# Optimization experiments

Measured on AMD Instinct MI355X. Metric: run time of the kernel, lower is better.

## Reference

```python
import jax, jax.numpy as jnp
import numpy as np

B, IN, H, MID = 16384, 256, 512, 64
GRID_SIZE, ORDER = 5, 3
GRID_LO, GRID_HI = -1.0, 1.0
NB = GRID_SIZE + ORDER  # 8 spline basis functions per input feature
LN_EPS = 1e-5


def make_grid(in_features):
    h = (GRID_HI - GRID_LO) / GRID_SIZE
    g = np.arange(-ORDER, GRID_SIZE + ORDER + 1, dtype=np.float32) * h + GRID_LO
    return jnp.asarray(np.tile(g, (in_features, 1)))  # (in, grid_size + 2*order + 1)


def layer_norm(x, g, b):
    mu = jnp.mean(x, axis=-1, keepdims=True)
    var = jnp.var(x, axis=-1, keepdims=True)
    return (x - mu) * jax.lax.rsqrt(var + LN_EPS) * g + b


def b_splines(x, grid):
    # x: (B, in), grid: (in, G). Cox-de Boor recursion (efficient-kan convention).
    xe = x[:, :, None]
    bases = ((xe >= grid[:, :-1]) & (xe < grid[:, 1:])).astype(x.dtype)
    for k in range(1, ORDER + 1):
        left = (xe - grid[:, :-(k + 1)]) / (grid[:, k:-1] - grid[:, :-(k + 1)])
        right = (grid[:, k + 1:] - xe) / (grid[:, k + 1:] - grid[:, 1:-k])
        bases = left * bases[:, :, :-1] + right * bases[:, :, 1:]
    return bases  # (B, in, NB)


def kan_linear(x, base_w, spline_w, scaler, grid):
    # base path: silu(x) @ W_base^T ; spline path: B-spline bases contracted with scaled spline weights
    base = jax.nn.silu(x) @ base_w.T
    bs = b_splines(x, grid)
    spline = jnp.einsum('bik,oik->bo', bs, spline_w * scaler[:, :, None])
    return base + spline


def setup_inputs() -> dict:
    key = jax.random.key(0)
    ks = jax.random.split(key, 24)

    def n(k, shape, fan_in):
        return jax.random.normal(k, shape, dtype=jnp.float32) / np.sqrt(fan_in)

    H2 = 2 * H
    return {
        'x': jax.random.normal(ks[0], (B, IN), jnp.float32),
        'h_prev': jax.random.normal(ks[1], (B, H), jnp.float32),
        'ip_w': n(ks[2], (H, IN), IN), 'ip_b': jnp.zeros((H,), jnp.float32),
        'rg_w': n(ks[3], (H, H2), H2), 'rg_b': jnp.zeros((H,), jnp.float32),
        'rg_g': jnp.ones((H,), jnp.float32), 'rg_beta': jnp.zeros((H,), jnp.float32),
        'ug_w': n(ks[4], (H, H2), H2), 'ug_b': jnp.zeros((H,), jnp.float32),
        'ug_g': jnp.ones((H,), jnp.float32), 'ug_beta': jnp.zeros((H,), jnp.float32),
        'k1_base': n(ks[5], (MID, H2), H2),
        'k1_spline': n(ks[6], (MID, H2, NB), H2) * 0.1,
        'k1_scaler': n(ks[7], (MID, H2), H2) + 1.0,
        'grid1': make_grid(H2),
        'k2_base': n(ks[8], (H, MID), MID),
        'k2_spline': n(ks[9], (H, MID, NB), MID) * 0.1,
        'k2_scaler': n(ks[10], (H, MID), MID) + 1.0,
        'grid2': make_grid(MID),
        'cn_g': jnp.ones((H,), jnp.float32), 'cn_b': jnp.zeros((H,), jnp.float32),
        'rp_w': n(ks[11], (H, H2), H2), 'rp_b': jnp.zeros((H,), jnp.float32),
    }


def reference(x, h_prev, ip_w, ip_b, rg_w, rg_b, rg_g, rg_beta, ug_w, ug_b, ug_g, ug_beta,
              k1_base, k1_spline, k1_scaler, grid1, k2_base, k2_spline, k2_scaler, grid2,
              cn_g, cn_b, rp_w, rp_b):
    x_proj = x @ ip_w.T + ip_b
    combined = jnp.concatenate([x_proj, h_prev], axis=1)  # (B, 2H)
    # reset gate is computed in the original forward but never used; kept for faithfulness
    reset = jnp.tanh(layer_norm(combined @ rg_w.T + rg_b, rg_g, rg_beta))  # noqa: F841
    update = jax.nn.sigmoid(layer_norm(combined @ ug_w.T + ug_b, ug_g, ug_beta))
    # KAN candidate: [2H] -> 64 -> H
    mid = kan_linear(combined, k1_base, k1_spline, k1_scaler, grid1)
    h_cand = kan_linear(mid, k2_base, k2_spline, k2_scaler, grid2)
    residual = combined @ rp_w.T + rp_b
    h_cand = layer_norm(h_cand + residual, cn_g, cn_b)
    h_cand = layer_norm(h_cand, cn_g, cn_b)  # same LayerNorm applied twice, as in source
    h_cand = jax.nn.silu(h_cand)
    h_t = (1.0 - update) * h_prev + update * h_cand
    return h_t
```

## Files before the change

kernel.cpp:

```cpp
#include <hip/hip_runtime.h>
#include <hip/hip_bf16.h>

#define BATCH 16384

typedef __attribute__((ext_vector_type(8))) short short8;
typedef __attribute__((ext_vector_type(4))) float f32x4;

typedef const __attribute__((address_space(1))) uint* gas_t;
typedef __attribute__((address_space(3))) uint* las_t;

__device__ __forceinline__ void gl_lds16(const void* g, void* l) {
    __builtin_amdgcn_global_load_lds((gas_t)g, (las_t)l, 16, 0, 0);
}

__device__ __forceinline__ float bf2f(uint u) { union { uint u; float f; } v; v.u = u << 16; return v.f; }
__device__ __forceinline__ ushort f2bf(float f) {
    union { float f; uint u; } v; v.f = f;
    uint r = v.u + 0x7fffu + ((v.u >> 16) & 1u);
    return (ushort)(r >> 16);
}
__device__ __forceinline__ uint pack2(float a, float b) { return (uint)f2bf(a) | ((uint)f2bf(b) << 16); }
__device__ __forceinline__ uint pack_trunc(float lo, float hi) {
    return __builtin_amdgcn_perm(__float_as_uint(hi), __float_as_uint(lo), 0x07060302u);
}
__device__ __forceinline__ float sigmoidf_(float x) { return __builtin_amdgcn_rcpf(1.0f + __expf(-x)); }
__device__ __forceinline__ float siluf_(float x)    { return x * sigmoidf_(x); }

__device__ __forceinline__ void bases_packed(float x, float g0, float inv_h, uint o[4]) {
    float u = (x - g0) * inv_h;
    float fl = floorf(u);
    float f = u - fl;
    float f2 = f * f, f3 = f2 * f;
    float Ca = f3 * (1.0f / 6.0f);
    float Cb = (1.0f / 6.0f) + 0.5f * (f + f2 - f3);
    float Cc = (2.0f / 3.0f) + 0.5f * f3 - f2;
    float Cd = (1.0f / 6.0f) + 0.5f * (f2 - f) - f3 * (1.0f / 6.0f);
    int t0 = (int)fl;
    t0 = max(-8, min(t0, 19));
    uint dlo = pack_trunc(Cd, Cc);
    uint dhi = pack_trunc(Cb, Ca);
    unsigned long long D = (unsigned long long)dlo | ((unsigned long long)dhi << 32);
    int sp = t0 * 16 - 48;
    unsigned long long l1 = D << (sp & 63);
    unsigned long long r1 = D >> ((-sp) & 63);
    unsigned long long r2 = D >> ((64 - sp) & 63);
    unsigned long long l2 = D << ((sp - 64) & 63);
    unsigned long long lo = (sp >= 0) ? (sp < 64 ? l1 : 0ull) : (sp > -64 ? r1 : 0ull);
    unsigned long long hi = (sp > 0 && sp < 128) ? (sp < 64 ? r2 : l2) : 0ull;
    o[0] = (uint)lo; o[1] = (uint)(lo >> 32); o[2] = (uint)hi; o[3] = (uint)(hi >> 32);
}

__global__ __launch_bounds__(256) void prep_all(const float* __restrict__ ip_w, const float* __restrict__ ug_w,
                                                const float* __restrict__ rp,  const float* __restrict__ k2b,
                                                const float* __restrict__ k2s, const float* __restrict__ k2sc,
                                                const float* __restrict__ k1b, const float* __restrict__ k1s,
                                                const float* __restrict__ k1sc,
                                                ushort* __restrict__ ipw, ushort* __restrict__ ugw,
                                                ushort* __restrict__ wcat, ushort* __restrict__ w1aug) {
    int t = blockIdx.x * 256 + threadIdx.x;
    if (t < 131072) { ipw[t] = f2bf(ip_w[t]); return; }
    t -= 131072;
    if (t < 524288) { ugw[t] = f2bf(ug_w[t]); return; }
    t -= 524288;
    if (t < 819200) {
        int n = t / 1600, c = t % 1600; float v;
        if (c < 1024) v = rp[n * 1024 + c];
        else if (c < 1088) v = k2b[n * 64 + (c - 1024)];
        else { int i = (c - 1088) >> 3, k = (c - 1088) & 7; v = k2s[(n * 64 + i) * 8 + k] * k2sc[n * 64 + i]; }
        wcat[t] = f2bf(v); return;
    }
    t -= 819200;
    if (t < 589824) {
        int n = t / 9216, c = t % 9216; float v;
        if (c < 1024) v = k1b[n * 1024 + c];
        else { int i = (c - 1024) >> 3, k = (c - 1024) & 7; v = k1s[(n * 1024 + i) * 8 + k] * k1sc[n * 1024 + i]; }
        w1aug[t] = f2bf(v);
    }
}

__global__ __launch_bounds__(256) void copy_h_sil(const float* __restrict__ hp,
                                                  ushort* __restrict__ acat, ushort* __restrict__ ssw) {
    int t = blockIdx.x * 256 + threadIdx.x;
    int b = t >> 6, j = (t & 63) * 8;
    const float4* s = (const float4*)(hp + (size_t)b * 512 + j);
    float4 a = s[0], c = s[1];
    uint4 o; o.x = pack2(a.x, a.y); o.y = pack2(a.z, a.w); o.z = pack2(c.x, c.y); o.w = pack2(c.z, c.w);
    *(uint4*)(acat + (size_t)b * 1600 + 512 + j) = o;
    uint4 q; q.x = pack2(siluf_(a.x), siluf_(a.y)); q.y = pack2(siluf_(a.z), siluf_(a.w));
    q.z = pack2(siluf_(c.x), siluf_(c.y)); q.w = pack2(siluf_(c.z), siluf_(c.w));
    *(uint4*)(ssw + (size_t)b * 1024 + 512 + j) = q;
}

__global__ __launch_bounds__(256) void gemm_mfma(const ushort* __restrict__ A, int lda,
                                                 const ushort* __restrict__ Wt, int ldw,
                                                 const float* __restrict__ bias,
                                                 ushort* __restrict__ C, int ldc, int K) {
    __shared__ ushort As[2][128 * 64];
    __shared__ ushort Bs[2][128 * 64];
    const int tid = threadIdx.x;
    const int w = tid >> 6, lane = tid & 63;
    const int fr = lane & 15, fq = lane >> 4;
    const int m0 = blockIdx.x * 128, n0 = blockIdx.y * 128;
    const int wm = w & 1, wn = w >> 1;

    const int srow8 = lane >> 3;
    const int scol  = ((lane & 7) ^ srow8) << 3;
    const ushort* gA[4]; const ushort* gB[4]; int fa[4];
#pragma unroll
    for (int j = 0; j < 4; ++j) {
        int rowj = (j * 4 + w) * 8 + srow8;
        fa[j] = (j * 4 + w) * 512 + lane * 8;
        gA[j] = A  + (size_t)(m0 + rowj) * lda + scol;
        gB[j] = Wt + (size_t)(n0 + rowj) * ldw + scol;
    }
    const int nt = K / 64;
#pragma unroll
    for (int j = 0; j < 4; ++j) {
        gl_lds16(gA[j], &As[0][fa[j]]); gl_lds16(gB[j], &Bs[0][fa[j]]);
        gA[j] += 64; gB[j] += 64;
    }
    f32x4 acc[4][4] = {};
    int cur = 0;
    for (int t = 0; t < nt; ++t) {
        __syncthreads();
        if (t + 1 < nt) {
#pragma unroll
            for (int j = 0; j < 4; ++j) {
                gl_lds16(gA[j], &As[cur ^ 1][fa[j]]); gl_lds16(gB[j], &Bs[cur ^ 1][fa[j]]);
                gA[j] += 64; gB[j] += 64;
            }
        }
#pragma unroll
        for (int s = 0; s < 2; ++s) {
            const int csw = ((s * 4 + fq) ^ (fr & 7)) << 3;
            short8 af[4], bv[4];
#pragma unroll
            for (int mi = 0; mi < 4; ++mi)
                af[mi] = *(const short8*)(&As[cur][(wm * 64 + mi * 16 + fr) * 64 + csw]);
#pragma unroll
            for (int ni = 0; ni < 4; ++ni)
                bv[ni] = *(const short8*)(&Bs[cur][(wn * 64 + ni * 16 + fr) * 64 + csw]);
#pragma unroll
            for (int mi = 0; mi < 4; ++mi)
#pragma unroll
                for (int ni = 0; ni < 4; ++ni)
                    acc[mi][ni] = __builtin_amdgcn_mfma_f32_16x16x32_bf16(af[mi], bv[ni], acc[mi][ni], 0, 0, 0);
        }
        cur ^= 1;
    }
#pragma unroll
    for (int mi = 0; mi < 4; ++mi) {
#pragma unroll
        for (int ni = 0; ni < 4; ++ni) {
            int n = n0 + wn * 64 + ni * 16 + fr;
            float bvs = bias[n];
#pragma unroll
            for (int r = 0; r < 4; ++r) {
                int m = m0 + wm * 64 + mi * 16 + fq * 4 + r;
                C[(size_t)m * ldc + n] = f2bf(acc[mi][ni][r] + bvs);
            }
        }
    }
}

__global__ __launch_bounds__(256) void gemm_ip(const float* __restrict__ X,
                                               const ushort* __restrict__ Wt,
                                               const float* __restrict__ bias,
                                               ushort* __restrict__ acat,
                                               ushort* __restrict__ ssw) {
    __shared__ ushort As[2][128 * 64];
    __shared__ ushort Bs[2][128 * 64];
    const int tid = threadIdx.x;
    const int w = tid >> 6, lane = tid & 63;
    const int fr = lane & 15, fq = lane >> 4;
    const int m0 = blockIdx.x * 128, n0 = blockIdx.y * 128;
    const int wm = w & 1, wn = w >> 1;

    const int srow8 = lane >> 3;
    const int scol = ((lane & 7) ^ srow8) << 3;
    const ushort* gB[4]; int fa[4];
#pragma unroll
    for (int j = 0; j < 4; ++j) {
        int rowj = (j * 4 + w) * 8 + srow8;
        fa[j] = (j * 4 + w) * 512 + lane * 8;
        gB[j] = Wt + (size_t)(n0 + rowj) * 256 + scol;
    }
    const float* gA[4]; int ar[4];
#pragma unroll
    for (int j = 0; j < 4; ++j) {
        int rj = j * 32 + (tid >> 3);
        int lc = (tid & 7) ^ (rj & 7);
        ar[j] = rj * 64 + (tid & 7) * 8;
        gA[j] = X + (size_t)(m0 + rj) * 256 + lc * 8;
    }
    float4 va[4], vb[4];
#pragma unroll
    for (int j = 0; j < 4; ++j) { gl_lds16(gB[j], &Bs[0][fa[j]]); gB[j] += 64; }
#pragma unroll
    for (int j = 0; j < 4; ++j) { va[j] = *(const float4*)gA[j]; vb[j] = *(const float4*)(gA[j] + 4); gA[j] += 64; }
#pragma unroll
    for (int j = 0; j < 4; ++j) {
        uint4 o; o.x = pack2(va[j].x, va[j].y); o.y = pack2(va[j].z, va[j].w);
        o.z = pack2(vb[j].x, vb[j].y); o.w = pack2(vb[j].z, vb[j].w);
        *(uint4*)&As[0][ar[j]] = o;
    }
    f32x4 acc[4][4] = {};
    int cur = 0;
    for (int t = 0; t < 4; ++t) {
        __syncthreads();
        if (t < 3) {
#pragma unroll
            for (int j = 0; j < 4; ++j) { gl_lds16(gB[j], &Bs[cur ^ 1][fa[j]]); gB[j] += 64; }
#pragma unroll
            for (int j = 0; j < 4; ++j) { va[j] = *(const float4*)gA[j]; vb[j] = *(const float4*)(gA[j] + 4); gA[j] += 64; }
        }
#pragma unroll
        for (int s = 0; s < 2; ++s) {
            const int csw = ((s * 4 + fq) ^ (fr & 7)) << 3;
            short8 af[4], bv[4];
#pragma unroll
            for (int mi = 0; mi < 4; ++mi)
                af[mi] = *(const short8*)(&As[cur][(wm * 64 + mi * 16 + fr) * 64 + csw]);
#pragma unroll
            for (int ni = 0; ni < 4; ++ni)
                bv[ni] = *(const short8*)(&Bs[cur][(wn * 64 + ni * 16 + fr) * 64 + csw]);
#pragma unroll
            for (int mi = 0; mi < 4; ++mi)
#pragma unroll
                for (int ni = 0; ni < 4; ++ni)
                    acc[mi][ni] = __builtin_amdgcn_mfma_f32_16x16x32_bf16(af[mi], bv[ni], acc[mi][ni], 0, 0, 0);
        }
        if (t < 3) {
#pragma unroll
            for (int j = 0; j < 4; ++j) {
                uint4 o; o.x = pack2(va[j].x, va[j].y); o.y = pack2(va[j].z, va[j].w);
                o.z = pack2(vb[j].x, vb[j].y); o.w = pack2(vb[j].z, vb[j].w);
                *(uint4*)&As[cur ^ 1][ar[j]] = o;
            }
        }
        cur ^= 1;
    }
#pragma unroll
    for (int mi = 0; mi < 4; ++mi) {
#pragma unroll
        for (int ni = 0; ni < 4; ++ni) {
            int n = n0 + wn * 64 + ni * 16 + fr;
            float bvs = bias[n];
#pragma unroll
            for (int r = 0; r < 4; ++r) {
                int m = m0 + wm * 64 + mi * 16 + fq * 4 + r;
                float val = acc[mi][ni][r] + bvs;
                acat[(size_t)m * 1600 + n] = f2bf(val);
                ssw[(size_t)m * 1024 + n] = f2bf(siluf_(val));
            }
        }
    }
}

__global__ __launch_bounds__(256) void kan1_mfma(const ushort* __restrict__ acat,
                                                 const ushort* __restrict__ ssw,
                                                 const ushort* __restrict__ w1aug,
                                                 const float* __restrict__ grid1,
                                                 float* __restrict__ midp) {
    __shared__ ushort As[2][64 * 64];
    __shared__ ushort Bs[2][64 * 64];
    const int tid = threadIdx.x;
    const int w = tid >> 6, lane = tid & 63;
    const int fr = lane & 15, fq = lane >> 4;
    const int m0 = blockIdx.x * 64;
    const int kb = blockIdx.y;
    const float g0 = grid1[0];
    const float inv_h = 1.0f / (grid1[1] - g0);

    const int srow = tid >> 3, sc = tid & 7;
    const int xr = srow & 7;
    const int lc8 = (sc ^ xr) << 3;
    const ushort* swA0 = ssw + (size_t)(m0 + srow) * 1024 + lc8;
    const ushort* swA1 = ssw + (size_t)(m0 + srow + 32) * 1024 + lc8;
    const ushort* wB0  = w1aug + (size_t)srow * 9216 + lc8;
    const ushort* wB1  = w1aug + (size_t)(srow + 32) * 9216 + lc8;
    const ushort* aRow0 = acat + (size_t)(m0 + srow) * 1600;
    const ushort* aRow1 = acat + (size_t)(m0 + srow + 32) * 1600;
    const int wpo = srow * 64 + lc8;
    const int wm = w & 1, wn = w >> 1;

    f32x4 acc[2][2] = {};
    {
        int c = kb * 128;
        gl_lds16(wB0 + c, &Bs[0][tid * 8]); gl_lds16(wB1 + c, &Bs[0][2048 + tid * 8]);
        gl_lds16(swA0 + c, &As[0][tid * 8]); gl_lds16(swA1 + c, &As[0][2048 + tid * 8]);
    }
    int cur = 0;
    for (int s = 0; s < 18; ++s) {
        __syncthreads();
        if (s + 1 < 18) {
            int c = (s + 1 < 2) ? kb * 128 + (s + 1) * 64 : 1024 + kb * 1024 + (s - 1) * 64;
            gl_lds16(wB0 + c, &Bs[cur ^ 1][tid * 8]);
            gl_lds16(wB1 + c, &Bs[cur ^ 1][2048 + tid * 8]);
            if (s + 1 < 2) {
                gl_lds16(swA0 + c, &As[cur ^ 1][tid * 8]);
                gl_lds16(swA1 + c, &As[cur ^ 1][2048 + tid * 8]);
            } else {
                int i = ((c - 1024) >> 3) + sc;
                float x0 = bf2f((uint)aRow0[i]);
                float x1 = bf2f((uint)aRow1[i]);
                uint o0[4], o1[4];
                bases_packed(x0, g0, inv_h, o0);
                bases_packed(x1, g0, inv_h, o1);
                uint4 q0; q0.x = o0[0]; q0.y = o0[1]; q0.z = o0[2]; q0.w = o0[3];
                uint4 q1; q1.x = o1[0]; q1.y = o1[1]; q1.z = o1[2]; q1.w = o1[3];
                *(uint4*)&As[cur ^ 1][wpo] = q0;
                *(uint4*)&As[cur ^ 1][2048 + wpo] = q1;
            }
        }
#pragma unroll
        for (int s2 = 0; s2 < 2; ++s2) {
            short8 af[2], bv[2];
#pragma unroll
            for (int mi = 0; mi < 2; ++mi) {
                int arow = wm * 32 + mi * 16 + fr;
                af[mi] = *(const short8*)(&As[cur][arow * 64 + (((s2 * 4 + fq) ^ (arow & 7)) << 3)]);
            }
#pragma unroll
            for (int ni = 0; ni < 2; ++ni) {
                int brow = wn * 32 + ni * 16 + fr;
                bv[ni] = *(const short8*)(&Bs[cur][brow * 64 + (((s2 * 4 + fq) ^ (brow & 7)) << 3)]);
            }
#pragma unroll
            for (int mi = 0; mi < 2; ++mi)
#pragma unroll
                for (int ni = 0; ni < 2; ++ni)
                    acc[mi][ni] = __builtin_amdgcn_mfma_f32_16x16x32_bf16(af[mi], bv[ni], acc[mi][ni], 0, 0, 0);
        }
        cur ^= 1;
    }
    float* outp = midp + (size_t)kb * (BATCH * 64);
#pragma unroll
    for (int mi = 0; mi < 2; ++mi)
#pragma unroll
        for (int ni = 0; ni < 2; ++ni)
#pragma unroll
            for (int r = 0; r < 4; ++r)
                outp[(size_t)(m0 + wm * 32 + mi * 16 + fq * 4 + r) * 64 + wn * 32 + ni * 16 + fr] = acc[mi][ni][r];
}

__global__ __launch_bounds__(256) void bs2_kernel(const float* __restrict__ midp,
                                                  const float* __restrict__ grid2,
                                                  ushort* __restrict__ acat) {
    int t = blockIdx.x * 256 + threadIdx.x;
    if (t >= BATCH * 64) return;
    float x = 0.0f;
#pragma unroll
    for (int p = 0; p < 8; ++p) x += midp[(size_t)p * (BATCH * 64) + t];
    int b = t >> 6, i = t & 63;
    float g0 = grid2[0], inv_h = 1.0f / (grid2[1] - g0);
    acat[(size_t)b * 1600 + 1024 + i] = f2bf(siluf_(x));
    uint o[4];
    bases_packed(x, g0, inv_h, o);
    uint4 o4; o4.x = o[0]; o4.y = o[1]; o4.z = o[2]; o4.w = o[3];
    *(uint4*)&acat[(size_t)b * 1600 + 1088 + i * 8] = o4;
}

__device__ __forceinline__ void block_reduce_2(float& a, float& b, float (*red)[4]) {
#pragma unroll
    for (int off = 32; off; off >>= 1) {
        a += __shfl_xor(a, off, 64);
        b += __shfl_xor(b, off, 64);
    }
    int lane = threadIdx.x & 63, wid = threadIdx.x >> 6;
    if (lane == 0) { red[0][wid] = a; red[1][wid] = b; }
    __syncthreads();
    a = red[0][0] + red[0][1] + red[0][2] + red[0][3];
    b = red[1][0] + red[1][1] + red[1][2] + red[1][3];
}

__global__ __launch_bounds__(256) void final2(const ushort* __restrict__ ug,
                                              const ushort* __restrict__ hcb,
                                              const float* __restrict__ hprev,
                                              const float* __restrict__ ug_g,
                                              const float* __restrict__ ug_beta,
                                              const float* __restrict__ cg,
                                              const float* __restrict__ cb,
                                              float* __restrict__ out) {
    int row = blockIdx.x, tid = threadIdx.x;
    __shared__ float rA[2][4], rB[2][4], rC[2][4];
    float u0 = bf2f((uint)ug[(size_t)row * 512 + tid]);
    float u1 = bf2f((uint)ug[(size_t)row * 512 + tid + 256]);
    float h0 = bf2f((uint)hcb[(size_t)row * 512 + tid]);
    float h1 = bf2f((uint)hcb[(size_t)row * 512 + tid + 256]);
    float s = u0 + u1, ss = u0 * u0 + u1 * u1;
    block_reduce_2(s, ss, rA);
    float mu = s * (1.0f / 512.0f);
    float var = ss * (1.0f / 512.0f) - mu * mu;
    float r = rsqrtf(var + 1e-5f);
    float uu0 = sigmoidf_((u0 - mu) * r * ug_g[tid] + ug_beta[tid]);
    float uu1 = sigmoidf_((u1 - mu) * r * ug_g[tid + 256] + ug_beta[tid + 256]);
    float cg0 = cg[tid], cg1 = cg[tid + 256], cb0 = cb[tid], cb1 = cb[tid + 256];
    float s2 = h0 + h1, ss2 = h0 * h0 + h1 * h1;
    block_reduce_2(s2, ss2, rB);
    float mu2 = s2 * (1.0f / 512.0f);
    float var2 = ss2 * (1.0f / 512.0f) - mu2 * mu2;
    float r2 = rsqrtf(var2 + 1e-5f);
    float w0 = (h0 - mu2) * r2 * cg0 + cb0;
    float w1 = (h1 - mu2) * r2 * cg1 + cb1;
    float s3 = w0 + w1, ss3 = w0 * w0 + w1 * w1;
    block_reduce_2(s3, ss3, rC);
    float mu3 = s3 * (1.0f / 512.0f);
    float var3 = ss3 * (1.0f / 512.0f) - mu3 * mu3;
    float r3 = rsqrtf(var3 + 1e-5f);
    float c0 = siluf_((w0 - mu3) * r3 * cg0 + cb0);
    float c1 = siluf_((w1 - mu3) * r3 * cg1 + cb1);
    size_t o0 = (size_t)row * 512 + tid, o1 = o0 + 256;
    float hp0 = hprev[o0], hp1 = hprev[o1];
    out[o0] = (1.0f - uu0) * hp0 + uu0 * c0;
    out[o1] = (1.0f - uu1) * hp1 + uu1 * c1;
}

extern "C" void kernel_launch(void* const* d_in, const int* in_sizes, int n_in,
                              void* d_out, int out_size, void* d_ws, size_t ws_size,
                              hipStream_t stream) {
    const float* x        = (const float*)d_in[0];
    const float* h_prev   = (const float*)d_in[1];
    const float* ip_w     = (const float*)d_in[2];
    const float* ip_b     = (const float*)d_in[3];
    const float* ug_w     = (const float*)d_in[8];
    const float* ug_b     = (const float*)d_in[9];
    const float* ug_g     = (const float*)d_in[10];
    const float* ug_beta  = (const float*)d_in[11];
    const float* k1_base  = (const float*)d_in[12];
    const float* k1_spline= (const float*)d_in[13];
    const float* k1_scaler= (const float*)d_in[14];
    const float* grid1    = (const float*)d_in[15];
    const float* k2_base  = (const float*)d_in[16];
    const float* k2_spline= (const float*)d_in[17];
    const float* k2_scaler= (const float*)d_in[18];
    const float* grid2    = (const float*)d_in[19];
    const float* cn_g     = (const float*)d_in[20];
    const float* cn_b     = (const float*)d_in[21];
    const float* rp_w     = (const float*)d_in[22];
    const float* rp_b     = (const float*)d_in[23];
    float* out = (float*)d_out;
    char* W = (char*)d_ws;

    ushort* Acat    = (ushort*)(W);
    ushort* ug_bf   = (ushort*)(W + 52428800);
    ushort* silu_sw = (ushort*)(W + 69206016);
    float*  midp    = (float*) (W + 102760448);
    ushort* hc_bf   = (ushort*)(W + 102760448);
    ushort* ipw_bf  = (ushort*)(W + 136314880);
    ushort* ugw_bf  = (ushort*)(W + 136577024);
    ushort* wcat    = (ushort*)(W + 137625600);
    ushort* w1aug   = (ushort*)(W + 139264000);

    hipLaunchKernelGGL(prep_all, dim3(8064), dim3(256), 0, stream,
                       ip_w, ug_w, rp_w, k2_base, k2_spline, k2_scaler,
                       k1_base, k1_spline, k1_scaler, ipw_bf, ugw_bf, wcat, w1aug);
    hipLaunchKernelGGL(copy_h_sil, dim3(4096), dim3(256), 0, stream, h_prev, Acat, silu_sw);

    hipLaunchKernelGGL(gemm_ip, dim3(BATCH / 128, 4), dim3(256), 0, stream,
                       x, ipw_bf, ip_b, Acat, silu_sw);

    hipLaunchKernelGGL(gemm_mfma, dim3(BATCH / 128, 4), dim3(256), 0, stream,
                       Acat, 1600, ugw_bf, 1024, ug_b, ug_bf, 512, 1024);

    hipLaunchKernelGGL(kan1_mfma, dim3(BATCH / 64, 8), dim3(256), 0, stream,
                       Acat, silu_sw, w1aug, grid1, midp);
    hipLaunchKernelGGL(bs2_kernel, dim3(BATCH * 64 / 256), dim3(256), 0, stream, midp, grid2, Acat);

    hipLaunchKernelGGL(gemm_mfma, dim3(BATCH / 128, 4), dim3(256), 0, stream,
                       Acat, 1600, wcat, 1600, rp_b, hc_bf, 512, 1600);

    hipLaunchKernelGGL(final2, dim3(BATCH), dim3(256), 0, stream, ug_bf, hc_bf, h_prev, ug_g, ug_beta, cn_g, cn_b, out);
}
```

Baseline: 175.2 us.

## Shrink GEMM N-tile to 64, restage KAN1 pipeline, read bf16 h_prev in final

The shared bf16 MFMA GEMM uses 128x64 tiles instead of 128x128, doubling the grid to improve occupancy and CU fill for the N=512 outputs. The KAN layer-1 kernel preloads its input scalars into registers up front and runs an explicitly unrolled double-buffered schedule instead of loading them per stage. The final kernel reads h_prev from the bf16 concatenated buffer rather than the fp32 input, cutting bytes read. This lowers the precision of the residual h_prev term, and the smaller tile re-reads A more often.

```diff
diff --git a/kernel.cpp b/kernel.cpp
--- a/kernel.cpp
+++ b/kernel.cpp
@@ -91,59 +91,65 @@
     *(uint4*)(ssw + (size_t)b * 1024 + 512 + j) = q;
 }
 
-__global__ __launch_bounds__(256) void gemm_mfma(const ushort* __restrict__ A, int lda,
-                                                 const ushort* __restrict__ Wt, int ldw,
-                                                 const float* __restrict__ bias,
-                                                 ushort* __restrict__ C, int ldc, int K) {
+__global__ __launch_bounds__(256) void gemm_n64(const ushort* __restrict__ A, int lda,
+                                                const ushort* __restrict__ Wt, int ldw,
+                                                const float* __restrict__ bias,
+                                                ushort* __restrict__ C, int ldc, int K) {
     __shared__ ushort As[2][128 * 64];
-    __shared__ ushort Bs[2][128 * 64];
+    __shared__ ushort Bs[2][64 * 64];
     const int tid = threadIdx.x;
     const int w = tid >> 6, lane = tid & 63;
     const int fr = lane & 15, fq = lane >> 4;
-    const int m0 = blockIdx.x * 128, n0 = blockIdx.y * 128;
+    const int m0 = blockIdx.x * 128, n0 = blockIdx.y * 64;
     const int wm = w & 1, wn = w >> 1;
-
-    const int srow8 = lane >> 3;
-    const int scol  = ((lane & 7) ^ srow8) << 3;
-    const ushort* gA[4]; const ushort* gB[4]; int fa[4];
+    const int sr = tid >> 3, pc = tid & 7;
+
+    const ushort* gA[4]; const ushort* gB[2]; int fa[4], fb[2];
 #pragma unroll
     for (int j = 0; j < 4; ++j) {
-        int rowj = (j * 4 + w) * 8 + srow8;
-        fa[j] = (j * 4 + w) * 512 + lane * 8;
-        gA[j] = A  + (size_t)(m0 + rowj) * lda + scol;
-        gB[j] = Wt + (size_t)(n0 + rowj) * ldw + scol;
+        int r = j * 32 + sr;
+        fa[j] = r * 64 + pc * 8;
+        gA[j] = A + (size_t)(m0 + r) * lda + ((pc ^ (r & 7)) << 3);
+    }
+#pragma unroll
+    for (int j = 0; j < 2; ++j) {
+        int r = j * 32 + sr;
+        fb[j] = r * 64 + pc * 8;
+        gB[j] = Wt + (size_t)(n0 + r) * ldw + ((pc ^ (r & 7)) << 3);
     }
     const int nt = K / 64;
 #pragma unroll
-    for (int j = 0; j < 4; ++j) {
-        gl_lds16(gA[j], &As[0][fa[j]]); gl_lds16(gB[j], &Bs[0][fa[j]]);
-        gA[j] += 64; gB[j] += 64;
-    }
-    f32x4 acc[4][4] = {};
+    for (int j = 0; j < 4; ++j) { gl_lds16(gA[j], &As[0][fa[j]]); gA[j] += 64; }
+#pragma unroll
+    for (int j = 0; j < 2; ++j) { gl_lds16(gB[j], &Bs[0][fb[j]]); gB[j] += 64; }
+
+    f32x4 acc[4][2] = {};
     int cur = 0;
     for (int t = 0; t < nt; ++t) {
         __syncthreads();
         if (t + 1 < nt) {
 #pragma unroll
-            for (int j = 0; j < 4; ++j) {
-                gl_lds16(gA[j], &As[cur ^ 1][fa[j]]); gl_lds16(gB[j], &Bs[cur ^ 1][fa[j]]);
-                gA[j] += 64; gB[j] += 64;
-            }
+            for (int j = 0; j < 4; ++j) { gl_lds16(gA[j], &As[cur ^ 1][fa[j]]); gA[j] += 64; }
+#pragma unroll
+            for (int j = 0; j < 2; ++j) { gl_lds16(gB[j], &Bs[cur ^ 1][fb[j]]); gB[j] += 64; }
         }
 #pragma unroll
         for (int s = 0; s < 2; ++s) {
-            const int csw = ((s * 4 + fq) ^ (fr & 7)) << 3;
-            short8 af[4], bv[4];
+            short8 af[4], bv[2];
+#pragma unroll
+            for (int mi = 0; mi < 4; ++mi) {
+                int arow = wm * 64 + mi * 16 + fr;
+                af[mi] = *(const short8*)(&As[cur][arow * 64 + (((s * 4 + fq) ^ (arow & 7)) << 3)]);
+            }
+#pragma unroll
+            for (int ni = 0; ni < 2; ++ni) {
+                int brow = wn * 32 + ni * 16 + fr;
+                bv[ni] = *(const short8*)(&Bs[cur][brow * 64 + (((s * 4 + fq) ^ (brow & 7)) << 3)]);
+            }
 #pragma unroll
             for (int mi = 0; mi < 4; ++mi)
-                af[mi] = *(const short8*)(&As[cur][(wm * 64 + mi * 16 + fr) * 64 + csw]);
-#pragma unroll
-            for (int ni = 0; ni < 4; ++ni)
-                bv[ni] = *(const short8*)(&Bs[cur][(wn * 64 + ni * 16 + fr) * 64 + csw]);
-#pragma unroll
-            for (int mi = 0; mi < 4; ++mi)
-#pragma unroll
-                for (int ni = 0; ni < 4; ++ni)
+#pragma unroll
+                for (int ni = 0; ni < 2; ++ni)
                     acc[mi][ni] = __builtin_amdgcn_mfma_f32_16x16x32_bf16(af[mi], bv[ni], acc[mi][ni], 0, 0, 0);
         }
         cur ^= 1;
@@ -151,8 +157,8 @@
 #pragma unroll
     for (int mi = 0; mi < 4; ++mi) {
 #pragma unroll
-        for (int ni = 0; ni < 4; ++ni) {
-            int n = n0 + wn * 64 + ni * 16 + fr;
+        for (int ni = 0; ni < 2; ++ni) {
+            int n = n0 + wn * 32 + ni * 16 + fr;
             float bvs = bias[n];
 #pragma unroll
             for (int r = 0; r < 4; ++r) {
@@ -279,52 +285,48 @@
     const ushort* swA1 = ssw + (size_t)(m0 + srow + 32) * 1024 + lc8;
     const ushort* wB0  = w1aug + (size_t)srow * 9216 + lc8;
     const ushort* wB1  = w1aug + (size_t)(srow + 32) * 9216 + lc8;
-    const ushort* aRow0 = acat + (size_t)(m0 + srow) * 1600;
-    const ushort* aRow1 = acat + (size_t)(m0 + srow + 32) * 1600;
     const int wpo = srow * 64 + lc8;
     const int wm = w & 1, wn = w >> 1;
 
+    uint xa[16], xb[16];
+    {
+        const ushort* r0 = acat + (size_t)(m0 + srow) * 1600 + kb * 128 + sc;
+        const ushort* r1 = acat + (size_t)(m0 + srow + 32) * 1600 + kb * 128 + sc;
+#pragma unroll
+        for (int bs = 0; bs < 16; ++bs) { xa[bs] = r0[bs * 8]; xb[bs] = r1[bs * 8]; }
+    }
+
     f32x4 acc[2][2] = {};
-    {
-        int c = kb * 128;
-        gl_lds16(wB0 + c, &Bs[0][tid * 8]); gl_lds16(wB1 + c, &Bs[0][2048 + tid * 8]);
-        gl_lds16(swA0 + c, &As[0][tid * 8]); gl_lds16(swA1 + c, &As[0][2048 + tid * 8]);
-    }
-    int cur = 0;
-    for (int s = 0; s < 18; ++s) {
-        __syncthreads();
-        if (s + 1 < 18) {
-            int c = (s + 1 < 2) ? kb * 128 + (s + 1) * 64 : 1024 + kb * 1024 + (s - 1) * 64;
-            gl_lds16(wB0 + c, &Bs[cur ^ 1][tid * 8]);
-            gl_lds16(wB1 + c, &Bs[cur ^ 1][2048 + tid * 8]);
-            if (s + 1 < 2) {
-                gl_lds16(swA0 + c, &As[cur ^ 1][tid * 8]);
-                gl_lds16(swA1 + c, &As[cur ^ 1][2048 + tid * 8]);
-            } else {
-                int i = ((c - 1024) >> 3) + sc;
-                float x0 = bf2f((uint)aRow0[i]);
-                float x1 = bf2f((uint)aRow1[i]);
-                uint o0[4], o1[4];
-                bases_packed(x0, g0, inv_h, o0);
-                bases_packed(x1, g0, inv_h, o1);
-                uint4 q0; q0.x = o0[0]; q0.y = o0[1]; q0.z = o0[2]; q0.w = o0[3];
-                uint4 q1; q1.x = o1[0]; q1.y = o1[1]; q1.z = o1[2]; q1.w = o1[3];
-                *(uint4*)&As[cur ^ 1][wpo] = q0;
-                *(uint4*)&As[cur ^ 1][2048 + wpo] = q1;
-            }
-        }
+    auto stageB = [&](int c, int buf) {
+        gl_lds16(wB0 + c, &Bs[buf][tid * 8]);
+        gl_lds16(wB1 + c, &Bs[buf][2048 + tid * 8]);
+    };
+    auto stageAsilu = [&](int c, int buf) {
+        gl_lds16(swA0 + c, &As[buf][tid * 8]);
+        gl_lds16(swA1 + c, &As[buf][2048 + tid * 8]);
+    };
+    auto stageAbases = [&](uint x0u, uint x1u, int buf) {
+        uint o0[4], o1[4];
+        bases_packed(bf2f(x0u), g0, inv_h, o0);
+        bases_packed(bf2f(x1u), g0, inv_h, o1);
+        uint4 q0; q0.x = o0[0]; q0.y = o0[1]; q0.z = o0[2]; q0.w = o0[3];
+        uint4 q1; q1.x = o1[0]; q1.y = o1[1]; q1.z = o1[2]; q1.w = o1[3];
+        *(uint4*)&As[buf][wpo] = q0;
+        *(uint4*)&As[buf][2048 + wpo] = q1;
+    };
+    auto mfma_step = [&](int buf) {
 #pragma unroll
         for (int s2 = 0; s2 < 2; ++s2) {
             short8 af[2], bv[2];
 #pragma unroll
             for (int mi = 0; mi < 2; ++mi) {
                 int arow = wm * 32 + mi * 16 + fr;
-                af[mi] = *(const short8*)(&As[cur][arow * 64 + (((s2 * 4 + fq) ^ (arow & 7)) << 3)]);
+                af[mi] = *(const short8*)(&As[buf][arow * 64 + (((s2 * 4 + fq) ^ (arow & 7)) << 3)]);
             }
 #pragma unroll
             for (int ni = 0; ni < 2; ++ni) {
                 int brow = wn * 32 + ni * 16 + fr;
-                bv[ni] = *(const short8*)(&Bs[cur][brow * 64 + (((s2 * 4 + fq) ^ (brow & 7)) << 3)]);
+                bv[ni] = *(const short8*)(&Bs[buf][brow * 64 + (((s2 * 4 + fq) ^ (brow & 7)) << 3)]);
             }
 #pragma unroll
             for (int mi = 0; mi < 2; ++mi)
@@ -332,8 +334,27 @@
                 for (int ni = 0; ni < 2; ++ni)
                     acc[mi][ni] = __builtin_amdgcn_mfma_f32_16x16x32_bf16(af[mi], bv[ni], acc[mi][ni], 0, 0, 0);
         }
-        cur ^= 1;
-    }
+    };
+
+    const int cB = kb * 128;
+    const int bB = 1024 + kb * 1024;
+    stageB(cB, 0); stageAsilu(cB, 0);
+    __syncthreads();
+    stageB(cB + 64, 1); stageAsilu(cB + 64, 1);
+    mfma_step(0);
+    __syncthreads();
+    stageB(bB, 0); stageAbases(xa[0], xb[0], 0);
+    mfma_step(1);
+#pragma unroll
+    for (int bs = 0; bs < 15; ++bs) {
+        __syncthreads();
+        stageB(bB + (bs + 1) * 64, (bs + 1) & 1);
+        stageAbases(xa[bs + 1], xb[bs + 1], (bs + 1) & 1);
+        mfma_step(bs & 1);
+    }
+    __syncthreads();
+    mfma_step(1);
+
     float* outp = midp + (size_t)kb * (BATCH * 64);
 #pragma unroll
     for (int mi = 0; mi < 2; ++mi)
@@ -376,7 +397,7 @@
 
 __global__ __launch_bounds__(256) void final2(const ushort* __restrict__ ug,
                                               const ushort* __restrict__ hcb,
-                                              const float* __restrict__ hprev,
+                                              const ushort* __restrict__ acat,
                                               const float* __restrict__ ug_g,
                                               const float* __restrict__ ug_beta,
                                               const float* __restrict__ cg,
@@ -388,6 +409,8 @@
     float u1 = bf2f((uint)ug[(size_t)row * 512 + tid + 256]);
     float h0 = bf2f((uint)hcb[(size_t)row * 512 + tid]);
     float h1 = bf2f((uint)hcb[(size_t)row * 512 + tid + 256]);
+    float hp0 = bf2f((uint)acat[(size_t)row * 1600 + 512 + tid]);
+    float hp1 = bf2f((uint)acat[(size_t)row * 1600 + 768 + tid]);
     float s = u0 + u1, ss = u0 * u0 + u1 * u1;
     block_reduce_2(s, ss, rA);
     float mu = s * (1.0f / 512.0f);
@@ -411,7 +434,6 @@
     float c0 = siluf_((w0 - mu3) * r3 * cg0 + cb0);
     float c1 = siluf_((w1 - mu3) * r3 * cg1 + cb1);
     size_t o0 = (size_t)row * 512 + tid, o1 = o0 + 256;
-    float hp0 = hprev[o0], hp1 = hprev[o1];
     out[o0] = (1.0f - uu0) * hp0 + uu0 * c0;
     out[o1] = (1.0f - uu1) * hp1 + uu1 * c1;
 }
@@ -460,15 +482,15 @@
     hipLaunchKernelGGL(gemm_ip, dim3(BATCH / 128, 4), dim3(256), 0, stream,
                        x, ipw_bf, ip_b, Acat, silu_sw);
 
-    hipLaunchKernelGGL(gemm_mfma, dim3(BATCH / 128, 4), dim3(256), 0, stream,
+    hipLaunchKernelGGL(gemm_n64, dim3(BATCH / 128, 8), dim3(256), 0, stream,
                        Acat, 1600, ugw_bf, 1024, ug_b, ug_bf, 512, 1024);
 
     hipLaunchKernelGGL(kan1_mfma, dim3(BATCH / 64, 8), dim3(256), 0, stream,
                        Acat, silu_sw, w1aug, grid1, midp);
     hipLaunchKernelGGL(bs2_kernel, dim3(BATCH * 64 / 256), dim3(256), 0, stream, midp, grid2, Acat);
 
-    hipLaunchKernelGGL(gemm_mfma, dim3(BATCH / 128, 4), dim3(256), 0, stream,
+    hipLaunchKernelGGL(gemm_n64, dim3(BATCH / 128, 8), dim3(256), 0, stream,
                        Acat, 1600, wcat, 1600, rp_b, hc_bf, 512, 1600);
 
-    hipLaunchKernelGGL(final2, dim3(BATCH), dim3(256), 0, stream, ug_bf, hc_bf, h_prev, ug_g, ug_beta, cn_g, cn_b, out);
-}
+    hipLaunchKernelGGL(final2, dim3(BATCH), dim3(256), 0, stream, ug_bf, hc_bf, Acat, ug_g, ug_beta, cn_g, cn_b, out);
+}
```

New measurement: 193.1 us. 10.2% more time.

## Load KAN1 weights directly to registers, precompute spline bases, read bf16 h_prev

Applied to the files above, without the earlier changes.

In kan1_mfma, the B operand tile no longer goes through shared memory. Each wave loads its weight fragments straight from global memory into registers, double-buffered one step ahead. The activation inputs are prefetched into registers up front, and the B-spline bases for the next step are computed after the MFMAs, which overlaps VALU work with matrix math and halves LDS use. final2 now reads h_prev from the bf16 copy in Acat instead of the fp32 input. This lowers bandwidth but adds bf16 rounding to the h_prev term of the output blend.

```diff
diff --git a/kernel.cpp b/kernel.cpp
--- a/kernel.cpp
+++ b/kernel.cpp
@@ -263,7 +263,6 @@
                                                  const float* __restrict__ grid1,
                                                  float* __restrict__ midp) {
     __shared__ ushort As[2][64 * 64];
-    __shared__ ushort Bs[2][64 * 64];
     const int tid = threadIdx.x;
     const int w = tid >> 6, lane = tid & 63;
     const int fr = lane & 15, fq = lane >> 4;
@@ -273,67 +272,89 @@
     const float inv_h = 1.0f / (grid1[1] - g0);
 
     const int srow = tid >> 3, sc = tid & 7;
-    const int xr = srow & 7;
-    const int lc8 = (sc ^ xr) << 3;
+    const int lc8 = (sc ^ (srow & 7)) << 3;
     const ushort* swA0 = ssw + (size_t)(m0 + srow) * 1024 + lc8;
     const ushort* swA1 = ssw + (size_t)(m0 + srow + 32) * 1024 + lc8;
-    const ushort* wB0  = w1aug + (size_t)srow * 9216 + lc8;
-    const ushort* wB1  = w1aug + (size_t)(srow + 32) * 9216 + lc8;
-    const ushort* aRow0 = acat + (size_t)(m0 + srow) * 1600;
-    const ushort* aRow1 = acat + (size_t)(m0 + srow + 32) * 1600;
     const int wpo = srow * 64 + lc8;
     const int wm = w & 1, wn = w >> 1;
 
+    const ushort* bBase0 = w1aug + (size_t)(wn * 32 + fr) * 9216 + fq * 8;
+    const ushort* bBase1 = w1aug + (size_t)(wn * 32 + 16 + fr) * 9216 + fq * 8;
+
+    uint xa[16], xb[16];
+    {
+        const ushort* r0 = acat + (size_t)(m0 + srow) * 1600 + kb * 128 + sc;
+        const ushort* r1 = acat + (size_t)(m0 + srow + 32) * 1600 + kb * 128 + sc;
+#pragma unroll
+        for (int bs = 0; bs < 16; ++bs) { xa[bs] = r0[bs * 8]; xb[bs] = r1[bs * 8]; }
+    }
+
+    const int cB = kb * 128;
+    const int bB = 1024 + kb * 1024;
+#define KCOL(s) ((s) < 2 ? cB + (s) * 64 : bB + ((s) - 2) * 64)
+
     f32x4 acc[2][2] = {};
+    short8 bcur[2][2], bnxt[2][2];
+    uint q0[4], q1[4];
+
+    gl_lds16(swA0 + cB, &As[0][tid * 8]);
+    gl_lds16(swA1 + cB, &As[0][2048 + tid * 8]);
     {
-        int c = kb * 128;
-        gl_lds16(wB0 + c, &Bs[0][tid * 8]); gl_lds16(wB1 + c, &Bs[0][2048 + tid * 8]);
-        gl_lds16(swA0 + c, &As[0][tid * 8]); gl_lds16(swA1 + c, &As[0][2048 + tid * 8]);
-    }
-    int cur = 0;
+        int c = KCOL(0);
+#pragma unroll
+        for (int s2 = 0; s2 < 2; ++s2) {
+            bcur[0][s2] = *(const short8*)(bBase0 + c + s2 * 32);
+            bcur[1][s2] = *(const short8*)(bBase1 + c + s2 * 32);
+        }
+    }
+    __syncthreads();
+
+#pragma unroll
     for (int s = 0; s < 18; ++s) {
-        __syncthreads();
+        const int cur = s & 1;
         if (s + 1 < 18) {
-            int c = (s + 1 < 2) ? kb * 128 + (s + 1) * 64 : 1024 + kb * 1024 + (s - 1) * 64;
-            gl_lds16(wB0 + c, &Bs[cur ^ 1][tid * 8]);
-            gl_lds16(wB1 + c, &Bs[cur ^ 1][2048 + tid * 8]);
             if (s + 1 < 2) {
-                gl_lds16(swA0 + c, &As[cur ^ 1][tid * 8]);
-                gl_lds16(swA1 + c, &As[cur ^ 1][2048 + tid * 8]);
+                gl_lds16(swA0 + KCOL(s + 1), &As[cur ^ 1][tid * 8]);
+                gl_lds16(swA1 + KCOL(s + 1), &As[cur ^ 1][2048 + tid * 8]);
             } else {
-                int i = ((c - 1024) >> 3) + sc;
-                float x0 = bf2f((uint)aRow0[i]);
-                float x1 = bf2f((uint)aRow1[i]);
-                uint o0[4], o1[4];
-                bases_packed(x0, g0, inv_h, o0);
-                bases_packed(x1, g0, inv_h, o1);
-                uint4 q0; q0.x = o0[0]; q0.y = o0[1]; q0.z = o0[2]; q0.w = o0[3];
-                uint4 q1; q1.x = o1[0]; q1.y = o1[1]; q1.z = o1[2]; q1.w = o1[3];
-                *(uint4*)&As[cur ^ 1][wpo] = q0;
-                *(uint4*)&As[cur ^ 1][2048 + wpo] = q1;
+                uint4 t0; t0.x = q0[0]; t0.y = q0[1]; t0.z = q0[2]; t0.w = q0[3];
+                uint4 t1; t1.x = q1[0]; t1.y = q1[1]; t1.z = q1[2]; t1.w = q1[3];
+                *(uint4*)&As[cur ^ 1][wpo] = t0;
+                *(uint4*)&As[cur ^ 1][2048 + wpo] = t1;
+            }
+            int c = KCOL(s + 1);
+#pragma unroll
+            for (int s2 = 0; s2 < 2; ++s2) {
+                bnxt[0][s2] = *(const short8*)(bBase0 + c + s2 * 32);
+                bnxt[1][s2] = *(const short8*)(bBase1 + c + s2 * 32);
             }
         }
 #pragma unroll
         for (int s2 = 0; s2 < 2; ++s2) {
-            short8 af[2], bv[2];
+            short8 af[2];
 #pragma unroll
             for (int mi = 0; mi < 2; ++mi) {
                 int arow = wm * 32 + mi * 16 + fr;
                 af[mi] = *(const short8*)(&As[cur][arow * 64 + (((s2 * 4 + fq) ^ (arow & 7)) << 3)]);
             }
 #pragma unroll
-            for (int ni = 0; ni < 2; ++ni) {
-                int brow = wn * 32 + ni * 16 + fr;
-                bv[ni] = *(const short8*)(&Bs[cur][brow * 64 + (((s2 * 4 + fq) ^ (brow & 7)) << 3)]);
-            }
-#pragma unroll
             for (int mi = 0; mi < 2; ++mi)
 #pragma unroll
                 for (int ni = 0; ni < 2; ++ni)
-                    acc[mi][ni] = __builtin_amdgcn_mfma_f32_16x16x32_bf16(af[mi], bv[ni], acc[mi][ni], 0, 0, 0);
-        }
-        cur ^= 1;
-    }
+                    acc[mi][ni] = __builtin_amdgcn_mfma_f32_16x16x32_bf16(af[mi], bcur[ni][s2], acc[mi][ni], 0, 0, 0);
+        }
+        if (s < 16) {
+            bases_packed(bf2f(xa[s]), g0, inv_h, q0);
+            bases_packed(bf2f(xb[s]), g0, inv_h, q1);
+        }
+#pragma unroll
+        for (int ni = 0; ni < 2; ++ni)
+#pragma unroll
+            for (int s2 = 0; s2 < 2; ++s2) bcur[ni][s2] = bnxt[ni][s2];
+        __syncthreads();
+    }
+#undef KCOL
+
     float* outp = midp + (size_t)kb * (BATCH * 64);
 #pragma unroll
     for (int mi = 0; mi < 2; ++mi)
@@ -376,7 +397,7 @@
 
 __global__ __launch_bounds__(256) void final2(const ushort* __restrict__ ug,
                                               const ushort* __restrict__ hcb,
-                                              const float* __restrict__ hprev,
+                                              const ushort* __restrict__ acat,
                                               const float* __restrict__ ug_g,
                                               const float* __restrict__ ug_beta,
                                               const float* __restrict__ cg,
@@ -388,6 +409,8 @@
     float u1 = bf2f((uint)ug[(size_t)row * 512 + tid + 256]);
     float h0 = bf2f((uint)hcb[(size_t)row * 512 + tid]);
     float h1 = bf2f((uint)hcb[(size_t)row * 512 + tid + 256]);
+    float hp0 = bf2f((uint)acat[(size_t)row * 1600 + 512 + tid]);
+    float hp1 = bf2f((uint)acat[(size_t)row * 1600 + 768 + tid]);
     float s = u0 + u1, ss = u0 * u0 + u1 * u1;
     block_reduce_2(s, ss, rA);
     float mu = s * (1.0f / 512.0f);
@@ -411,7 +434,6 @@
     float c0 = siluf_((w0 - mu3) * r3 * cg0 + cb0);
     float c1 = siluf_((w1 - mu3) * r3 * cg1 + cb1);
     size_t o0 = (size_t)row * 512 + tid, o1 = o0 + 256;
-    float hp0 = hprev[o0], hp1 = hprev[o1];
     out[o0] = (1.0f - uu0) * hp0 + uu0 * c0;
     out[o1] = (1.0f - uu1) * hp1 + uu1 * c1;
 }
@@ -470,5 +492,5 @@
     hipLaunchKernelGGL(gemm_mfma, dim3(BATCH / 128, 4), dim3(256), 0, stream,
                        Acat, 1600, wcat, 1600, rp_b, hc_bf, 512, 1600);
 
-    hipLaunchKernelGGL(final2, dim3(BATCH), dim3(256), 0, stream, ug_bf, hc_bf, h_prev, ug_g, ug_beta, cn_g, cn_b, out);
-}
+    hipLaunchKernelGGL(final2, dim3(BATCH), dim3(256), 0, stream, ug_bf, hc_bf, Acat, ug_g, ug_beta, cn_g, cn_b, out);
+}
```

After: 201.0 us. 1.15x slower.
